# Optimization experiments

Hardware: AMD Instinct MI355X
Metric: run time of the kernel (lower is better)

## Reference

```python
import jax, jax.numpy as jnp
import numpy as np

N = 50000        # total nodes (random mix of disease type=1 and mirna type=0)
E = 1250000      # edges, avg degree 25
D_SIM = 256      # similarity feature dim (G.ndata['d_sim']/['m_sim'] width)
F_ATTN = 64      # feature_attn_size
SLOPE = 0.2      # leaky_relu negative slope


def setup_inputs() -> dict:
    key = jax.random.key(0)
    k = jax.random.split(key, 7)
    d_sim = jax.random.normal(k[0], (N, D_SIM), dtype=jnp.float32)
    m_sim = jax.random.normal(k[1], (N, D_SIM), dtype=jnp.float32)
    node_type = jax.random.randint(k[2], (N,), 0, 2, dtype=jnp.int32)
    src = jax.random.randint(k[3], (E,), 0, N)
    dst = jax.random.randint(k[4], (E,), 0, N)
    # xavier_normal with gain = calculate_gain('relu') = sqrt(2)
    scale = np.float32(np.sqrt(2.0) * np.sqrt(2.0 / (D_SIM + F_ATTN)))
    W_d = jax.random.normal(k[5], (D_SIM, F_ATTN), dtype=jnp.float32) * scale
    W_m = jax.random.normal(k[6], (D_SIM, F_ATTN), dtype=jnp.float32) * scale
    return {"d_sim": d_sim, "m_sim": m_sim, "W_d": W_d, "W_m": W_m,
            "node_type": node_type, "src": src, "dst": dst}


def reference(d_sim, m_sim, W_d, W_m, node_type, src, dst):
    # type-specific linear projection (dropout=0 -> identity)
    z_d = d_sim @ W_d                       # [N, F]
    z_m = m_sim @ W_m                       # [N, F]
    z = jnp.where((node_type == 1)[:, None], z_d, z_m)  # [N, F]

    # edge attention: leaky_relu(<z_src, z_dst>)
    z_src = z[src]                          # [E, F]
    e = jnp.sum(z_src * z[dst], axis=1)     # [E]
    e = jax.nn.leaky_relu(e, negative_slope=SLOPE)

    # segment softmax over incoming edges of each dst node
    e_max = jax.ops.segment_max(e, dst, num_segments=N)          # [N]
    e_max = jnp.where(jnp.isfinite(e_max), e_max, 0.0)           # empty segments
    ex = jnp.exp(e - e_max[dst])                                 # [E]
    denom = jax.ops.segment_sum(ex, dst, num_segments=N)         # [N]
    alpha = ex / jnp.maximum(denom[dst], 1e-16)                  # [E]

    # softmax-weighted neighbor aggregation, then ELU
    h = jax.ops.segment_sum(alpha[:, None] * z_src, dst, num_segments=N)  # [N, F]
    return jax.nn.elu(h)
```

## Files before the change

### kernel.cpp

```cpp
#include <hip/hip_runtime.h>
#include <math.h>


#define F 64
#define TM 128
#define TK 64
#define BSH 7
#define NSORT 192
#define CAP 4096
#define HCAP 2048

__global__ void classify_kernel(const int* __restrict__ node_type, int* __restrict__ tcnt,
                                int* __restrict__ list0, int* __restrict__ list1, int n) {
    int i = blockIdx.x * 256 + threadIdx.x;
    if (i < n) {
        int lane = threadIdx.x & 63;
        int t = node_type[i];
        unsigned long long b1 = __ballot(t == 1);
        unsigned long long ba = __ballot(1);
        unsigned long long mlt = (1ull << lane) - 1ull;
        int r1 = __popcll(b1 & mlt);
        int r0 = __popcll(ba & ~b1 & mlt);
        int base0, base1;
        if (lane == 0) {
            base1 = atomicAdd(&tcnt[1], __popcll(b1));
            base0 = atomicAdd(&tcnt[0], __popcll(ba & ~b1));
        }
        base0 = __shfl(base0, 0, 64);
        base1 = __shfl(base1, 0, 64);
        if (t == 1) list1[base1 + r1] = i;
        else        list0[base0 + r0] = i;
    }
}

__global__ __launch_bounds__(256, 2)
void proj_gemm(const float* __restrict__ d_sim, const float* __restrict__ m_sim,
               const float* __restrict__ W_d, const float* __restrict__ W_m,
               const int* __restrict__ tcnt, const int* __restrict__ list0,
               const int* __restrict__ list1, float* __restrict__ z) {
    __shared__ float sA[TM][TK + 1];
    __shared__ float sW[TK][F];
    int ty = blockIdx.y;
    int cnt = tcnt[ty];
    int base = blockIdx.x * TM;
    if (base >= cnt) return;
    const int*   list = ty ? list1 : list0;
    const float* A    = ty ? d_sim : m_sim;
    const float* W    = ty ? W_d   : W_m;

    int rg = threadIdx.x >> 4;
    int cg = threadIdx.x & 15;

    int srow_node[8];
    #pragma unroll
    for (int j = 0; j < 8; j++) {
        int idx = (int)threadIdx.x + 256 * j;
        int li = base + (idx >> 4);
        if (li >= cnt) li = cnt - 1;
        srow_node[j] = list[li];
    }

    float acc[8][4] = {};
    for (int kc = 0; kc < 256; kc += TK) {
        __syncthreads();
        #pragma unroll
        for (int j = 0; j < 8; j++) {
            int idx = (int)threadIdx.x + 256 * j;
            int r = idx >> 4, f4 = idx & 15;
            float4 v = *(const float4*)(A + (size_t)srow_node[j] * 256 + kc + f4 * 4);
            sA[r][f4 * 4 + 0] = v.x;
            sA[r][f4 * 4 + 1] = v.y;
            sA[r][f4 * 4 + 2] = v.z;
            sA[r][f4 * 4 + 3] = v.w;
        }
        #pragma unroll
        for (int j = 0; j < 4; j++) {
            int idx = (int)threadIdx.x + 256 * j;
            int k = idx >> 4, f4 = idx & 15;
            float4 v = *(const float4*)(W + (size_t)(kc + k) * F + f4 * 4);
            *(float4*)&sW[k][f4 * 4] = v;
        }
        __syncthreads();
        #pragma unroll 4
        for (int k = 0; k < TK; k++) {
            float4 wv = *(const float4*)&sW[k][cg * 4];
            float a[8];
            #pragma unroll
            for (int i = 0; i < 8; i++) a[i] = sA[rg * 8 + i][k];
            #pragma unroll
            for (int i = 0; i < 8; i++) {
                acc[i][0] = fmaf(a[i], wv.x, acc[i][0]);
                acc[i][1] = fmaf(a[i], wv.y, acc[i][1]);
                acc[i][2] = fmaf(a[i], wv.z, acc[i][2]);
                acc[i][3] = fmaf(a[i], wv.w, acc[i][3]);
            }
        }
    }
    #pragma unroll
    for (int i = 0; i < 8; i++) {
        int li = base + rg * 8 + i;
        if (li < cnt) {
            int node = list[li];
            float4 v = {acc[i][0], acc[i][1], acc[i][2], acc[i][3]};
            *(float4*)(z + (size_t)node * F + cg * 4) = v;
        }
    }
}

__global__ __launch_bounds__(1024)
void bucket_scatter(const int* __restrict__ dst, const int* __restrict__ src,
                    int* __restrict__ bucket_count, int* __restrict__ bucket_data,
                    int e, int nbuk, int chunk) {
    __shared__ int hist[512], base[512], rk[512];
    for (int i = threadIdx.x; i < nbuk; i += 1024) { hist[i] = 0; rk[i] = 0; }
    __syncthreads();
    int beg = blockIdx.x * chunk, end = min(e, beg + chunk);
    for (int i = beg + (int)threadIdx.x; i < end; i += 1024)
        atomicAdd(&hist[dst[i] >> BSH], 1);
    __syncthreads();
    for (int i = threadIdx.x; i < nbuk; i += 1024)
        base[i] = hist[i] ? atomicAdd(&bucket_count[i], hist[i]) : 0;
    __syncthreads();
    for (int i = beg + (int)threadIdx.x; i < end; i += 1024) {
        int d = dst[i];
        int b = d >> BSH;
        int r = atomicAdd(&rk[b], 1);
        int pos = base[b] + r;
        if (pos < CAP)
            bucket_data[(size_t)b * CAP + pos] = ((d & 127) << 16) | src[i];
    }
}

__global__ __launch_bounds__(512)
void attn_fused(const float* __restrict__ z, const int* __restrict__ bucket_count,
                const int* __restrict__ bucket_data, float* __restrict__ out, int n) {
    __shared__ unsigned short ssrc[HCAP];
    __shared__ int cnt[64], excl[64], cur[64];
    int b = blockIdx.x >> 1;
    int h = blockIdx.x & 1;
    int dbase = (b << BSH) + h * 64;
    const int* __restrict__ bd = bucket_data + (size_t)b * CAP;
    int len = min(bucket_count[b], CAP);

    if (threadIdx.x < 64) { cnt[threadIdx.x] = 0; cur[threadIdx.x] = 0; }
    __syncthreads();
    for (int i = threadIdx.x; i < len; i += 512) {
        int dl = bd[i] >> 16;
        if ((dl >> 6) == h) atomicAdd(&cnt[dl & 63], 1);
    }
    __syncthreads();
    if (threadIdx.x < 64) {
        int v = cnt[threadIdx.x];
        int s = v;
        #pragma unroll
        for (int off = 1; off < 64; off <<= 1) {
            int t = __shfl_up(s, off, 64);
            if ((int)threadIdx.x >= off) s += t;
        }
        excl[threadIdx.x] = s - v;
    }
    __syncthreads();
    for (int i = threadIdx.x; i < len; i += 512) {
        int v = bd[i];
        int dl = v >> 16;
        if ((dl >> 6) == h) {
            int d6 = dl & 63;
            int r = atomicAdd(&cur[d6], 1);
            int pos = excl[d6] + r;
            if (pos < HCAP) ssrc[pos] = (unsigned short)(v & 0xFFFF);
        }
    }
    __syncthreads();

    int lane = threadIdx.x & 63;
    int wv = threadIdx.x >> 6;
    int g = lane >> 4, r = lane & 15;
    for (int k = 0; k < 8; k++) {
        int d6 = wv + 8 * k;
        int node = dbase + d6;
        if (node >= n) continue;
        int lbeg = excl[d6];
        int lcnt = cnt[d6];
        if (lbeg + lcnt > HCAP) lcnt = max(0, HCAP - lbeg);
        float4 zd = ((const float4*)(z + (size_t)node * F))[r];
        float m = -3.402823466e38f, l = 0.f;
        float4 acc = {0.f, 0.f, 0.f, 0.f};
        for (int j = 0; j < lcnt; j += 4) {
            int jj = j + g;
            int s = ssrc[lbeg + min(jj, lcnt - 1)];
            float4 zc = ((const float4*)(z + (size_t)s * F))[r];
            float p = fmaf(zc.x, zd.x, fmaf(zc.y, zd.y, fmaf(zc.z, zd.z, zc.w * zd.w)));
            p += __shfl_xor(p, 1, 64);
            p += __shfl_xor(p, 2, 64);
            p += __shfl_xor(p, 4, 64);
            p += __shfl_xor(p, 8, 64);
            float e = (p > 0.f) ? p : 0.2f * p;
            if (jj >= lcnt) e = -INFINITY;
            float t = __expf(-fabsf(e - m));
            bool gt = (e > m);
            float sc = gt ? t : 1.f;
            float w  = gt ? 1.f : t;
            m = gt ? e : m;
            l = fmaf(l, sc, w);
            acc.x = fmaf(acc.x, sc, w * zc.x);
            acc.y = fmaf(acc.y, sc, w * zc.y);
            acc.z = fmaf(acc.z, sc, w * zc.z);
            acc.w = fmaf(acc.w, sc, w * zc.w);
        }
        #pragma unroll
        for (int off = 16; off <= 32; off <<= 1) {
            float om = __shfl_xor(m, off, 64);
            float ol = __shfl_xor(l, off, 64);
            float4 oa;
            oa.x = __shfl_xor(acc.x, off, 64);
            oa.y = __shfl_xor(acc.y, off, 64);
            oa.z = __shfl_xor(acc.z, off, 64);
            oa.w = __shfl_xor(acc.w, off, 64);
            float t = __expf(-fabsf(m - om));
            bool gt = (om > m);
            float sc = gt ? t : 1.f;
            float so = gt ? 1.f : t;
            m = gt ? om : m;
            l = fmaf(l, sc, ol * so);
            acc.x = fmaf(acc.x, sc, oa.x * so);
            acc.y = fmaf(acc.y, sc, oa.y * so);
            acc.z = fmaf(acc.z, sc, oa.z * so);
            acc.w = fmaf(acc.w, sc, oa.w * so);
        }
        float inv = 1.f / fmaxf(l, 1e-16f);
        float4 o;
        o.x = acc.x * inv; o.y = acc.y * inv; o.z = acc.z * inv; o.w = acc.w * inv;
        o.x = (o.x > 0.f) ? o.x : (__expf(o.x) - 1.f);
        o.y = (o.y > 0.f) ? o.y : (__expf(o.y) - 1.f);
        o.z = (o.z > 0.f) ? o.z : (__expf(o.z) - 1.f);
        o.w = (o.w > 0.f) ? o.w : (__expf(o.w) - 1.f);
        if (g == 0) ((float4*)(out + (size_t)node * F))[r] = o;
    }
}

extern "C" void kernel_launch(void* const* d_in, const int* in_sizes, int n_in,
                              void* d_out, int out_size, void* d_ws, size_t ws_size,
                              hipStream_t stream) {
    const float* d_sim     = (const float*)d_in[0];
    const float* m_sim     = (const float*)d_in[1];
    const float* W_d       = (const float*)d_in[2];
    const float* W_m       = (const float*)d_in[3];
    const int*   node_type = (const int*)d_in[4];
    const int*   src       = (const int*)d_in[5];
    const int*   dst       = (const int*)d_in[6];
    float* out = (float*)d_out;

    const int N = in_sizes[4];
    const int E = in_sizes[5];
    const int NBUK = (N + 127) >> BSH;

    char* ws = (char*)d_ws;
    float* z      = (float*)ws;
    int*   tcnt   = (int*)(ws + (size_t)N * F * 4);
    int*   bcount = tcnt + 2;
    int*   list0  = bcount + 512;
    int*   list1  = list0 + N;
    int*   bdata  = list1 + N;

    hipMemsetAsync(tcnt, 0, (size_t)(2 + 512) * sizeof(int), stream);

    dim3 blk(256);
    classify_kernel<<<dim3((N + 255) / 256), blk, 0, stream>>>(node_type, tcnt, list0, list1, N);
    proj_gemm<<<dim3((N + TM - 1) / TM, 2), blk, 0, stream>>>(d_sim, m_sim, W_d, W_m,
                                                              tcnt, list0, list1, z);
    int chunk = (E + NSORT - 1) / NSORT;
    bucket_scatter<<<dim3(NSORT), dim3(1024), 0, stream>>>(dst, src, bcount, bdata, E, NBUK, chunk);
    attn_fused<<<dim3((N + 63) / 64), dim3(512), 0, stream>>>(z, bcount, bdata, out, N);
}
```

Baseline: 246.4 us.

## Merge projection GEMM and edge bucket scatter into one heterogeneous launch

The two independent stages, the type-specific projection GEMM and the dst-bucket edge scatter, now run in a single kernel. The first NSORT blocks do the scatter and the remaining blocks do the GEMM, sharing one LDS buffer, so the stages can overlap on the GPU and one launch is saved. The scatter blocks drop from 1024 to 256 threads, which gives each of them less parallelism and could lengthen the scatter's critical path. NSORT is also nudged to 188.

```diff
diff --git a/kernel.cpp b/kernel.cpp
--- a/kernel.cpp
+++ b/kernel.cpp
@@ -6,9 +6,11 @@
 #define TM 128
 #define TK 64
 #define BSH 7
-#define NSORT 192
+#define NSORT 188
 #define CAP 4096
 #define HCAP 2048
+
+#define PROJ_LDS (128 * (TK + 1) * 4 + TK * F * 4)
 
 __global__ void classify_kernel(const int* __restrict__ node_type, int* __restrict__ tcnt,
                                 int* __restrict__ list0, int* __restrict__ list1, int n) {
@@ -34,19 +36,51 @@
 }
 
 __global__ __launch_bounds__(256, 2)
-void proj_gemm(const float* __restrict__ d_sim, const float* __restrict__ m_sim,
-               const float* __restrict__ W_d, const float* __restrict__ W_m,
-               const int* __restrict__ tcnt, const int* __restrict__ list0,
-               const int* __restrict__ list1, float* __restrict__ z) {
-    __shared__ float sA[TM][TK + 1];
-    __shared__ float sW[TK][F];
-    int ty = blockIdx.y;
+void proj_scatter(const float* __restrict__ d_sim, const float* __restrict__ m_sim,
+                  const float* __restrict__ W_d, const float* __restrict__ W_m,
+                  const int* __restrict__ tcnt, const int* __restrict__ list0,
+                  const int* __restrict__ list1, float* __restrict__ z,
+                  const int* __restrict__ dst, const int* __restrict__ src,
+                  int* __restrict__ bucket_count, int* __restrict__ bucket_data,
+                  int e, int nbuk, int chunk) {
+    __shared__ __align__(16) char smem[PROJ_LDS];
+    int bid = blockIdx.x;
+
+    if (bid < NSORT) {
+        int* hist  = (int*)smem;
+        int* bbase = hist + 512;
+        int* rk    = bbase + 512;
+        for (int i = threadIdx.x; i < nbuk; i += 256) { hist[i] = 0; rk[i] = 0; }
+        __syncthreads();
+        int beg = bid * chunk, end = min(e, beg + chunk);
+        for (int i = beg + (int)threadIdx.x; i < end; i += 256)
+            atomicAdd(&hist[dst[i] >> BSH], 1);
+        __syncthreads();
+        for (int i = threadIdx.x; i < nbuk; i += 256)
+            bbase[i] = hist[i] ? atomicAdd(&bucket_count[i], hist[i]) : 0;
+        __syncthreads();
+        for (int i = beg + (int)threadIdx.x; i < end; i += 256) {
+            int d = dst[i];
+            int b = d >> BSH;
+            int r = atomicAdd(&rk[b], 1);
+            int pos = bbase[b] + r;
+            if (pos < CAP)
+                bucket_data[(size_t)b * CAP + pos] = ((d & 127) << 16) | src[i];
+        }
+        return;
+    }
+
+    int pb = bid - NSORT;
+    int ty = pb & 1;
     int cnt = tcnt[ty];
-    int base = blockIdx.x * TM;
+    int base = (pb >> 1) * TM;
     if (base >= cnt) return;
     const int*   list = ty ? list1 : list0;
     const float* A    = ty ? d_sim : m_sim;
     const float* W    = ty ? W_d   : W_m;
+
+    float (*sA)[TK + 1] = (float (*)[TK + 1])smem;
+    float (*sW)[F]      = (float (*)[F])(smem + 128 * (TK + 1) * 4);
 
     int rg = threadIdx.x >> 4;
     int cg = threadIdx.x & 15;
@@ -104,30 +138,6 @@
             float4 v = {acc[i][0], acc[i][1], acc[i][2], acc[i][3]};
             *(float4*)(z + (size_t)node * F + cg * 4) = v;
         }
-    }
-}
-
-__global__ __launch_bounds__(1024)
-void bucket_scatter(const int* __restrict__ dst, const int* __restrict__ src,
-                    int* __restrict__ bucket_count, int* __restrict__ bucket_data,
-                    int e, int nbuk, int chunk) {
-    __shared__ int hist[512], base[512], rk[512];
-    for (int i = threadIdx.x; i < nbuk; i += 1024) { hist[i] = 0; rk[i] = 0; }
-    __syncthreads();
-    int beg = blockIdx.x * chunk, end = min(e, beg + chunk);
-    for (int i = beg + (int)threadIdx.x; i < end; i += 1024)
-        atomicAdd(&hist[dst[i] >> BSH], 1);
-    __syncthreads();
-    for (int i = threadIdx.x; i < nbuk; i += 1024)
-        base[i] = hist[i] ? atomicAdd(&bucket_count[i], hist[i]) : 0;
-    __syncthreads();
-    for (int i = beg + (int)threadIdx.x; i < end; i += 1024) {
-        int d = dst[i];
-        int b = d >> BSH;
-        int r = atomicAdd(&rk[b], 1);
-        int pos = base[b] + r;
-        if (pos < CAP)
-            bucket_data[(size_t)b * CAP + pos] = ((d & 127) << 16) | src[i];
     }
 }
 
@@ -266,9 +276,12 @@
 
     dim3 blk(256);
     classify_kernel<<<dim3((N + 255) / 256), blk, 0, stream>>>(node_type, tcnt, list0, list1, N);
-    proj_gemm<<<dim3((N + TM - 1) / TM, 2), blk, 0, stream>>>(d_sim, m_sim, W_d, W_m,
-                                                              tcnt, list0, list1, z);
+
+    int pgrid = 2 * ((N + TM - 1) / TM);
     int chunk = (E + NSORT - 1) / NSORT;
-    bucket_scatter<<<dim3(NSORT), dim3(1024), 0, stream>>>(dst, src, bcount, bdata, E, NBUK, chunk);
+    proj_scatter<<<dim3(NSORT + pgrid), blk, 0, stream>>>(d_sim, m_sim, W_d, W_m,
+                                                          tcnt, list0, list1, z,
+                                                          dst, src, bcount, bdata,
+                                                          E, NBUK, chunk);
     attn_fused<<<dim3((N + 63) / 64), dim3(512), 0, stream>>>(z, bcount, bdata, out, N);
 }
```

Measured after the change: 237.8 us. 3.5% less time.
